# Kernel tuning notes

Hardware: AMD Instinct MI355X
Metric: run time of the kernel (lower is better)

Reference implementation:

```python
import jax, jax.numpy as jnp
import numpy as np

N_NODES = 100000


def _gat_conv(x, edge_index, W, att_src, att_dst, bias, concat):
    """PyG-style GATConv (eval mode, self-loops already in edge_index).
    x: [N, F_in], W: [F_in, H*C], att_*: [H, C], bias: [H*C] or [C].
    """
    N = x.shape[0]
    H, C = att_src.shape
    xl = (x @ W).reshape(N, H, C)                      # [N, H, C]
    a_src = jnp.einsum('nhc,hc->nh', xl, att_src)      # [N, H]
    a_dst = jnp.einsum('nhc,hc->nh', xl, att_dst)      # [N, H]
    src, dst = edge_index[0], edge_index[1]
    e = jax.nn.leaky_relu(a_src[src] + a_dst[dst], negative_slope=0.2)  # [E, H]
    # segment softmax over incoming edges per destination node
    e_max = jax.ops.segment_max(e, dst, num_segments=N)                 # [N, H]
    e_exp = jnp.exp(e - e_max[dst])                                     # [E, H]
    denom = jax.ops.segment_sum(e_exp, dst, num_segments=N)             # [N, H]
    alpha = e_exp / (denom[dst] + 1e-16)                                # [E, H]
    msg = xl[src] * alpha[:, :, None]                                   # [E, H, C]
    out = jax.ops.segment_sum(msg, dst, num_segments=N)                 # [N, H, C]
    out = out.reshape(N, H * C) if concat else out.mean(axis=1)
    return out + bias


def setup_inputs() -> dict:
    key = jax.random.key(0)
    ks = jax.random.split(key, 12)
    in_dim, hidden, heads, out_dim = 128, 16, 8, 64
    E = 1600000
    x = jax.random.normal(ks[0], (N_NODES, in_dim), dtype=jnp.float32)
    edge_index = jax.random.randint(ks[1], (2, E), 0, N_NODES, dtype=jnp.int32)
    s1 = 1.0 / np.sqrt(in_dim)
    s2 = 1.0 / np.sqrt(hidden * heads)
    return {
        'x': x,
        'edge_index': edge_index,
        'W1': jax.random.normal(ks[2], (in_dim, heads * hidden), dtype=jnp.float32) * s1,
        'att_src1': jax.random.normal(ks[3], (heads, hidden), dtype=jnp.float32) * 0.1,
        'att_dst1': jax.random.normal(ks[4], (heads, hidden), dtype=jnp.float32) * 0.1,
        'b1': jnp.zeros((heads * hidden,), dtype=jnp.float32),
        'W2': jax.random.normal(ks[5], (heads * hidden, out_dim), dtype=jnp.float32) * s2,
        'att_src2': jax.random.normal(ks[6], (1, out_dim), dtype=jnp.float32) * 0.1,
        'att_dst2': jax.random.normal(ks[7], (1, out_dim), dtype=jnp.float32) * 0.1,
        'b2': jnp.zeros((out_dim,), dtype=jnp.float32),
    }


def reference(x, edge_index, W1, att_src1, att_dst1, b1, W2, att_src2, att_dst2, b2):
    N = x.shape[0]
    # PyG GATConv default add_self_loops=True
    loops = jnp.tile(jnp.arange(N, dtype=edge_index.dtype), (2, 1))
    ei = jnp.concatenate([edge_index, loops], axis=1)
    h = _gat_conv(x, ei, W1, att_src1, att_dst1, b1, concat=True)
    h = jax.nn.elu(h)
    # dropout is identity in eval mode
    out = _gat_conv(h, ei, W2, att_src2, att_dst2, b2, concat=False)
    return out
```

## Files before the change

kernel.cpp:

```cpp
#include <hip/hip_runtime.h>
#include <cmath>

typedef _Float16 half8 __attribute__((ext_vector_type(8)));
typedef float f32x4 __attribute__((ext_vector_type(4)));

#define CAP 48

__device__ __forceinline__ float elu1(float v) {
    return v > 0.f ? v : (__expf(v) - 1.f);
}

__global__ __launch_bounds__(256) void k_scatter(
    const int* __restrict__ src, const int* __restrict__ dst,
    int* __restrict__ cnt, int* __restrict__ sorted, int E, int M, int npc)
{
    int color = blockIdx.x & 7;
    int lo = color * npc, hi = lo + npc;
    int nb = gridDim.x >> 3;
    size_t stride = (size_t)nb * 256;
    for (size_t e = (size_t)(blockIdx.x >> 3) * 256 + threadIdx.x; e < (size_t)M; e += stride) {
        int s, d;
        if (e < (size_t)E) { s = src[e]; d = dst[e]; } else { s = (int)(e - E); d = s; }
        if (d >= lo && d < hi) {
            int pos = atomicAdd(&cnt[d], 1);
            if (pos < CAP) sorted[(size_t)d * CAP + pos] = s;
        }
    }
}

__global__ __launch_bounds__(256) void k_gemm1(
    const float* __restrict__ x, const float* __restrict__ W,
    const float* __restrict__ att_s, const float* __restrict__ att_d,
    _Float16* __restrict__ xlh, float* __restrict__ a_s, float* __restrict__ a_d, int N)
{
    __shared__ _Float16 Wt[128 * 136];
    int t = threadIdx.x;
    for (int i = t; i < 128 * 128; i += 256) {
        int k = i >> 7, n = i & 127;
        Wt[n * 136 + k] = (_Float16)W[i];
    }
    __syncthreads();

    int wave = t >> 6, lane = t & 63;
    int cl = lane & 15, quad = lane >> 4;
    int arow = blockIdx.x * 64 + wave * 16 + cl;
    int rr = arow < N ? arow : N - 1;

    half8 af[4];
#pragma unroll
    for (int ks = 0; ks < 4; ks++) {
        const float4* p = (const float4*)(x + (size_t)rr * 128 + ks * 32 + quad * 8);
        float4 A = p[0], B = p[1];
        af[ks][0] = (_Float16)A.x; af[ks][1] = (_Float16)A.y;
        af[ks][2] = (_Float16)A.z; af[ks][3] = (_Float16)A.w;
        af[ks][4] = (_Float16)B.x; af[ks][5] = (_Float16)B.y;
        af[ks][6] = (_Float16)B.z; af[ks][7] = (_Float16)B.w;
    }

    f32x4 acc[8];
#pragma unroll
    for (int nt = 0; nt < 8; nt++) acc[nt] = (f32x4){0.f, 0.f, 0.f, 0.f};

#pragma unroll
    for (int nt = 0; nt < 8; nt++) {
        int n = nt * 16 + cl;
#pragma unroll
        for (int ks = 0; ks < 4; ks++) {
            half8 bf = *(const half8*)&Wt[n * 136 + ks * 32 + quad * 8];
            acc[nt] = __builtin_amdgcn_mfma_f32_16x16x32_f16(af[ks], bf, acc[nt], 0, 0, 0);
        }
    }

    float asl[8], adl[8];
#pragma unroll
    for (int nt = 0; nt < 8; nt++) {
        asl[nt] = att_s[nt * 16 + cl];
        adl[nt] = att_d[nt * 16 + cl];
    }

    int rbase = blockIdx.x * 64 + wave * 16 + quad * 4;
#pragma unroll
    for (int r = 0; r < 4; r++) {
        int orow = rbase + r;
        bool ok = orow < N;
#pragma unroll
        for (int nt = 0; nt < 8; nt++) {
            float v = acc[nt][r];
            if (ok) xlh[(size_t)orow * 128 + nt * 16 + cl] = (_Float16)v;
        }
#pragma unroll
        for (int nt = 0; nt < 8; nt++) {
            float ps = acc[nt][r] * asl[nt];
            float pd = acc[nt][r] * adl[nt];
            ps += __shfl_xor(ps, 1); ps += __shfl_xor(ps, 2);
            ps += __shfl_xor(ps, 4); ps += __shfl_xor(ps, 8);
            pd += __shfl_xor(pd, 1); pd += __shfl_xor(pd, 2);
            pd += __shfl_xor(pd, 4); pd += __shfl_xor(pd, 8);
            if (ok && cl == 0) {
                a_s[(size_t)orow * 8 + nt] = ps;
                a_d[(size_t)orow * 8 + nt] = pd;
            }
        }
    }
}

__global__ __launch_bounds__(256) void k_gemm2(
    const _Float16* __restrict__ h, const float* __restrict__ W,
    const float* __restrict__ att_s, const float* __restrict__ att_d,
    _Float16* __restrict__ xlh, float* __restrict__ a_s, float* __restrict__ a_d, int N)
{
    __shared__ _Float16 Wt[64 * 136];
    int t = threadIdx.x;
    for (int i = t; i < 128 * 64; i += 256) {
        int k = i >> 6, n = i & 63;
        Wt[n * 136 + k] = (_Float16)W[i];
    }
    __syncthreads();

    int wave = t >> 6, lane = t & 63;
    int cl = lane & 15, quad = lane >> 4;
    int arow = blockIdx.x * 64 + wave * 16 + cl;
    int rr = arow < N ? arow : N - 1;

    half8 af[4];
#pragma unroll
    for (int ks = 0; ks < 4; ks++)
        af[ks] = *(const half8*)(h + (size_t)rr * 128 + ks * 32 + quad * 8);

    f32x4 acc[4];
#pragma unroll
    for (int nt = 0; nt < 4; nt++) acc[nt] = (f32x4){0.f, 0.f, 0.f, 0.f};

#pragma unroll
    for (int nt = 0; nt < 4; nt++) {
        int n = nt * 16 + cl;
#pragma unroll
        for (int ks = 0; ks < 4; ks++) {
            half8 bf = *(const half8*)&Wt[n * 136 + ks * 32 + quad * 8];
            acc[nt] = __builtin_amdgcn_mfma_f32_16x16x32_f16(af[ks], bf, acc[nt], 0, 0, 0);
        }
    }

    float asl[4], adl[4];
#pragma unroll
    for (int nt = 0; nt < 4; nt++) {
        asl[nt] = att_s[nt * 16 + cl];
        adl[nt] = att_d[nt * 16 + cl];
    }

    int rbase = blockIdx.x * 64 + wave * 16 + quad * 4;
#pragma unroll
    for (int r = 0; r < 4; r++) {
        int orow = rbase + r;
        bool ok = orow < N;
        float ps = 0.f, pd = 0.f;
#pragma unroll
        for (int nt = 0; nt < 4; nt++) {
            float v = acc[nt][r];
            if (ok) xlh[(size_t)orow * 64 + nt * 16 + cl] = (_Float16)v;
            ps += v * asl[nt];
            pd += v * adl[nt];
        }
        ps += __shfl_xor(ps, 1); ps += __shfl_xor(ps, 2);
        ps += __shfl_xor(ps, 4); ps += __shfl_xor(ps, 8);
        pd += __shfl_xor(pd, 1); pd += __shfl_xor(pd, 2);
        pd += __shfl_xor(pd, 4); pd += __shfl_xor(pd, 8);
        if (ok && cl == 0) { a_s[orow] = ps; a_d[orow] = pd; }
    }
}

__global__ __launch_bounds__(256) void k_agg1(
    const int* __restrict__ cnt, const int* __restrict__ ss,
    const float* __restrict__ as, const float* __restrict__ ad,
    const _Float16* __restrict__ xlh, const float* __restrict__ b1,
    _Float16* __restrict__ h, int N)
{
    int t = threadIdx.x;
    int g = (blockIdx.x * 256 + t) >> 3;
    if (g >= N) return;
    int lane = t & 7;
    int c = lane * 16;
    int deg = cnt[g]; deg = deg < CAP ? deg : CAP;
    int start = g * CAP, end = start + deg;
    float adv = ad[(size_t)g * 8 + lane];

    float l = 0.f;
    float acc[16];
#pragma unroll
    for (int j = 0; j < 16; j++) acc[j] = 0.f;

    int i = start;
    for (; i + 2 <= end; i += 2) {
        int s0 = ss[i], s1 = ss[i + 1];
        float a0 = as[(size_t)s0 * 8 + lane];
        float a1 = as[(size_t)s1 * 8 + lane];
        const _Float16* p0 = xlh + (size_t)s0 * 128 + c;
        const _Float16* p1 = xlh + (size_t)s1 * 128 + c;
        half8 x0a = *(const half8*)p0, x0b = *(const half8*)(p0 + 8);
        half8 x1a = *(const half8*)p1, x1b = *(const half8*)(p1 + 8);
        float v0 = a0 + adv; v0 = v0 > 0.f ? v0 : 0.2f * v0;
        float v1 = a1 + adv; v1 = v1 > 0.f ? v1 : 0.2f * v1;
        float w0 = __expf(v0), w1 = __expf(v1);
        l += w0 + w1;
#pragma unroll
        for (int j = 0; j < 8; j++) {
            acc[j]     += (float)x0a[j] * w0 + (float)x1a[j] * w1;
            acc[j + 8] += (float)x0b[j] * w0 + (float)x1b[j] * w1;
        }
    }
    if (i < end) {
        int s0 = ss[i];
        float v0 = as[(size_t)s0 * 8 + lane] + adv;
        v0 = v0 > 0.f ? v0 : 0.2f * v0;
        float w0 = __expf(v0);
        l += w0;
        const _Float16* p0 = xlh + (size_t)s0 * 128 + c;
        half8 x0a = *(const half8*)p0, x0b = *(const half8*)(p0 + 8);
#pragma unroll
        for (int j = 0; j < 8; j++) {
            acc[j]     += (float)x0a[j] * w0;
            acc[j + 8] += (float)x0b[j] * w0;
        }
    }
    float inv = 1.f / (l + 1e-16f);
    float4 bq[4];
    bq[0] = *(const float4*)(b1 + c);
    bq[1] = *(const float4*)(b1 + c + 4);
    bq[2] = *(const float4*)(b1 + c + 8);
    bq[3] = *(const float4*)(b1 + c + 12);
    const float* bb = (const float*)bq;
    half8 o0, o1;
#pragma unroll
    for (int j = 0; j < 8; j++) {
        o0[j] = (_Float16)elu1(acc[j] * inv + bb[j]);
        o1[j] = (_Float16)elu1(acc[j + 8] * inv + bb[j + 8]);
    }
    *(half8*)(h + (size_t)g * 128 + c) = o0;
    *(half8*)(h + (size_t)g * 128 + c + 8) = o1;
}

__global__ __launch_bounds__(256) void k_agg2(
    const int* __restrict__ cnt, const int* __restrict__ ss,
    const float* __restrict__ as, const float* __restrict__ ad,
    const _Float16* __restrict__ xlh, const float* __restrict__ b2,
    float* __restrict__ out, int N)
{
    int t = threadIdx.x;
    int g = (blockIdx.x * 256 + t) >> 3;
    if (g >= N) return;
    int lane = t & 7;
    int c = lane * 8;
    int deg = cnt[g]; deg = deg < CAP ? deg : CAP;
    int start = g * CAP, end = start + deg;
    float adv = ad[g];

    float l = 0.f;
    float acc[8];
#pragma unroll
    for (int j = 0; j < 8; j++) acc[j] = 0.f;

    int i = start;
    for (; i + 4 <= end; i += 4) {
        int s0 = ss[i], s1 = ss[i + 1], s2 = ss[i + 2], s3 = ss[i + 3];
        float a0 = as[s0], a1 = as[s1], a2 = as[s2], a3 = as[s3];
        half8 x0 = *(const half8*)(xlh + (size_t)s0 * 64 + c);
        half8 x1 = *(const half8*)(xlh + (size_t)s1 * 64 + c);
        half8 x2 = *(const half8*)(xlh + (size_t)s2 * 64 + c);
        half8 x3 = *(const half8*)(xlh + (size_t)s3 * 64 + c);
        float v0 = a0 + adv; v0 = v0 > 0.f ? v0 : 0.2f * v0;
        float v1 = a1 + adv; v1 = v1 > 0.f ? v1 : 0.2f * v1;
        float v2 = a2 + adv; v2 = v2 > 0.f ? v2 : 0.2f * v2;
        float v3 = a3 + adv; v3 = v3 > 0.f ? v3 : 0.2f * v3;
        float w0 = __expf(v0), w1 = __expf(v1), w2 = __expf(v2), w3 = __expf(v3);
        l += (w0 + w1) + (w2 + w3);
#pragma unroll
        for (int j = 0; j < 8; j++)
            acc[j] += ((float)x0[j] * w0 + (float)x1[j] * w1)
                    + ((float)x2[j] * w2 + (float)x3[j] * w3);
    }
    for (; i < end; i++) {
        int s0 = ss[i];
        float v0 = as[s0] + adv;
        v0 = v0 > 0.f ? v0 : 0.2f * v0;
        float w0 = __expf(v0);
        l += w0;
        half8 x0 = *(const half8*)(xlh + (size_t)s0 * 64 + c);
#pragma unroll
        for (int j = 0; j < 8; j++) acc[j] += (float)x0[j] * w0;
    }
    float inv = 1.f / (l + 1e-16f);
    float4 b0 = *(const float4*)(b2 + c);
    float4 b4 = *(const float4*)(b2 + c + 4);
    float bb[8] = {b0.x, b0.y, b0.z, b0.w, b4.x, b4.y, b4.z, b4.w};
    float4 o0, o1;
    o0.x = acc[0] * inv + bb[0];
    o0.y = acc[1] * inv + bb[1];
    o0.z = acc[2] * inv + bb[2];
    o0.w = acc[3] * inv + bb[3];
    o1.x = acc[4] * inv + bb[4];
    o1.y = acc[5] * inv + bb[5];
    o1.z = acc[6] * inv + bb[6];
    o1.w = acc[7] * inv + bb[7];
    *(float4*)(out + (size_t)g * 64 + c) = o0;
    *(float4*)(out + (size_t)g * 64 + c + 4) = o1;
}

extern "C" void kernel_launch(void* const* d_in, const int* in_sizes, int n_in,
                              void* d_out, int out_size, void* d_ws, size_t ws_size,
                              hipStream_t stream) {
    const float* x   = (const float*)d_in[0];
    const int*   ei  = (const int*)  d_in[1];
    const float* W1  = (const float*)d_in[2];
    const float* as1 = (const float*)d_in[3];
    const float* ad1 = (const float*)d_in[4];
    const float* b1  = (const float*)d_in[5];
    const float* W2  = (const float*)d_in[6];
    const float* as2 = (const float*)d_in[7];
    const float* ad2 = (const float*)d_in[8];
    const float* b2  = (const float*)d_in[9];

    const int N = in_sizes[0] / 128;
    const int E = in_sizes[1] / 2;
    const int M = E + N;
    const int npc = (N + 7) / 8;
    const int SB = ((M + 256 * 8 - 1) / (256 * 8)) * 8;
    const int* src = ei;
    const int* dst = ei + E;

    float* ws    = (float*)d_ws;
    _Float16* xl1h = (_Float16*)ws;
    float* as1v  = ws   + (size_t)N * 64;
    float* ad1v  = as1v + (size_t)N * 8;
    _Float16* hbuf = (_Float16*)(ad1v + (size_t)N * 8);
    float* as2v  = ad1v + (size_t)N * 8 + (size_t)N * 64;
    float* ad2v  = as2v + (size_t)N;
    int*   cnt   = (int*)(ad2v + (size_t)N);
    int*   sorted= cnt + (size_t)N;
    _Float16* xl2h = xl1h;
    float* out   = (float*)d_out;

    size_t need = ((size_t)N * (147 + CAP)) * 4;
    if (ws_size < need) return;

    hipMemsetAsync(cnt, 0, (size_t)N * 4, stream);

    k_scatter<<<SB, 256, 0, stream>>>(src, dst, cnt, sorted, E, M, npc);
    k_gemm1  <<<(N + 63) / 64, 256, 0, stream>>>(x, W1, as1, ad1, xl1h, as1v, ad1v, N);

    k_agg1 <<<(int)(((size_t)N * 8 + 255) / 256), 256, 0, stream>>>(
        cnt, sorted, as1v, ad1v, xl1h, b1, hbuf, N);

    k_gemm2<<<(N + 63) / 64, 256, 0, stream>>>(hbuf, W2, as2, ad2, xl2h, as2v, ad2v, N);

    k_agg2 <<<(int)(((size_t)N * 8 + 255) / 256), 256, 0, stream>>>(
        cnt, sorted, as2v, ad2v, xl2h, b2, out, N);
}
```

Before: 350.4 us.

## Fuse layer-1 aggregation with layer-2 GEMM and fold counter reset into GEMM1

The layer-1 aggregation now writes its ELU output tile into shared memory, and the same block immediately runs the layer-2 MFMA projection and attention dot products. This removes the global round trip of the hidden activations and one kernel launch. The separate memset of the degree counters is replaced by zeroing inside k_gemm1, which now runs before the scatter. The cost is that every 32-node block reloads and converts W2 into LDS, and the fused kernel uses more LDS per block, which may lower occupancy for the latency-bound gather loop.

```diff
diff --git a/kernel.cpp b/kernel.cpp
--- a/kernel.cpp
+++ b/kernel.cpp
@@ -8,6 +8,86 @@
 
 __device__ __forceinline__ float elu1(float v) {
     return v > 0.f ? v : (__expf(v) - 1.f);
+}
+
+__global__ __launch_bounds__(256) void k_gemm1(
+    const float* __restrict__ x, const float* __restrict__ W,
+    const float* __restrict__ att_s, const float* __restrict__ att_d,
+    _Float16* __restrict__ xlh, float* __restrict__ a_s, float* __restrict__ a_d,
+    int* __restrict__ cnt, int N)
+{
+    __shared__ _Float16 Wt[128 * 136];
+    int t = threadIdx.x;
+
+    for (int i = blockIdx.x * 256 + t; i < N; i += gridDim.x * 256) cnt[i] = 0;
+
+    for (int i = t; i < 128 * 128; i += 256) {
+        int k = i >> 7, n = i & 127;
+        Wt[n * 136 + k] = (_Float16)W[i];
+    }
+    __syncthreads();
+
+    int wave = t >> 6, lane = t & 63;
+    int cl = lane & 15, quad = lane >> 4;
+    int arow = blockIdx.x * 64 + wave * 16 + cl;
+    int rr = arow < N ? arow : N - 1;
+
+    half8 af[4];
+#pragma unroll
+    for (int ks = 0; ks < 4; ks++) {
+        const float4* p = (const float4*)(x + (size_t)rr * 128 + ks * 32 + quad * 8);
+        float4 A = p[0], B = p[1];
+        af[ks][0] = (_Float16)A.x; af[ks][1] = (_Float16)A.y;
+        af[ks][2] = (_Float16)A.z; af[ks][3] = (_Float16)A.w;
+        af[ks][4] = (_Float16)B.x; af[ks][5] = (_Float16)B.y;
+        af[ks][6] = (_Float16)B.z; af[ks][7] = (_Float16)B.w;
+    }
+
+    f32x4 acc[8];
+#pragma unroll
+    for (int nt = 0; nt < 8; nt++) acc[nt] = (f32x4){0.f, 0.f, 0.f, 0.f};
+
+#pragma unroll
+    for (int nt = 0; nt < 8; nt++) {
+        int n = nt * 16 + cl;
+#pragma unroll
+        for (int ks = 0; ks < 4; ks++) {
+            half8 bf = *(const half8*)&Wt[n * 136 + ks * 32 + quad * 8];
+            acc[nt] = __builtin_amdgcn_mfma_f32_16x16x32_f16(af[ks], bf, acc[nt], 0, 0, 0);
+        }
+    }
+
+    float asl[8], adl[8];
+#pragma unroll
+    for (int nt = 0; nt < 8; nt++) {
+        asl[nt] = att_s[nt * 16 + cl];
+        adl[nt] = att_d[nt * 16 + cl];
+    }
+
+    int rbase = blockIdx.x * 64 + wave * 16 + quad * 4;
+#pragma unroll
+    for (int r = 0; r < 4; r++) {
+        int orow = rbase + r;
+        bool ok = orow < N;
+#pragma unroll
+        for (int nt = 0; nt < 8; nt++) {
+            float v = acc[nt][r];
+            if (ok) xlh[(size_t)orow * 128 + nt * 16 + cl] = (_Float16)v;
+        }
+#pragma unroll
+        for (int nt = 0; nt < 8; nt++) {
+            float ps = acc[nt][r] * asl[nt];
+            float pd = acc[nt][r] * adl[nt];
+            ps += __shfl_xor(ps, 1); ps += __shfl_xor(ps, 2);
+            ps += __shfl_xor(ps, 4); ps += __shfl_xor(ps, 8);
+            pd += __shfl_xor(pd, 1); pd += __shfl_xor(pd, 2);
+            pd += __shfl_xor(pd, 4); pd += __shfl_xor(pd, 8);
+            if (ok && cl == 0) {
+                a_s[(size_t)orow * 8 + nt] = ps;
+                a_d[(size_t)orow * 8 + nt] = pd;
+            }
+        }
+    }
 }
 
 __global__ __launch_bounds__(256) void k_scatter(
@@ -28,215 +108,144 @@
     }
 }
 
-__global__ __launch_bounds__(256) void k_gemm1(
-    const float* __restrict__ x, const float* __restrict__ W,
-    const float* __restrict__ att_s, const float* __restrict__ att_d,
-    _Float16* __restrict__ xlh, float* __restrict__ a_s, float* __restrict__ a_d, int N)
+__global__ __launch_bounds__(256) void k_agg1_gemm2(
+    const int* __restrict__ cnt, const int* __restrict__ ss,
+    const float* __restrict__ as, const float* __restrict__ ad,
+    const _Float16* __restrict__ xlh, const float* __restrict__ b1,
+    const float* __restrict__ W2,
+    const float* __restrict__ att_s2, const float* __restrict__ att_d2,
+    _Float16* __restrict__ xl2h, float* __restrict__ a_s2, float* __restrict__ a_d2, int N)
 {
-    __shared__ _Float16 Wt[128 * 136];
+    __shared__ _Float16 W2t[64 * 136];
+    __shared__ _Float16 Ht[32 * 136];
+    __shared__ float asb[2][32], adb[2][32];
+
     int t = threadIdx.x;
-    for (int i = t; i < 128 * 128; i += 256) {
-        int k = i >> 7, n = i & 127;
-        Wt[n * 136 + k] = (_Float16)W[i];
+
+    for (int i = t; i < 128 * 64; i += 256) {
+        int k = i >> 6, n = i & 63;
+        W2t[n * 136 + k] = (_Float16)W2[i];
+    }
+
+    int ln = t >> 3;
+    int g = blockIdx.x * 32 + ln;
+    int lane8 = t & 7;
+    int c = lane8 * 16;
+    {
+        int gg = g < N ? g : N - 1;
+        int deg = cnt[gg]; deg = deg < CAP ? deg : CAP;
+        int start = gg * CAP, end = start + deg;
+        float adv = ad[(size_t)gg * 8 + lane8];
+
+        float l = 0.f;
+        float acc[16];
+#pragma unroll
+        for (int j = 0; j < 16; j++) acc[j] = 0.f;
+
+        int i = start;
+        for (; i + 2 <= end; i += 2) {
+            int s0 = ss[i], s1 = ss[i + 1];
+            float a0 = as[(size_t)s0 * 8 + lane8];
+            float a1 = as[(size_t)s1 * 8 + lane8];
+            const _Float16* p0 = xlh + (size_t)s0 * 128 + c;
+            const _Float16* p1 = xlh + (size_t)s1 * 128 + c;
+            half8 x0a = *(const half8*)p0, x0b = *(const half8*)(p0 + 8);
+            half8 x1a = *(const half8*)p1, x1b = *(const half8*)(p1 + 8);
+            float v0 = a0 + adv; v0 = v0 > 0.f ? v0 : 0.2f * v0;
+            float v1 = a1 + adv; v1 = v1 > 0.f ? v1 : 0.2f * v1;
+            float w0 = __expf(v0), w1 = __expf(v1);
+            l += w0 + w1;
+#pragma unroll
+            for (int j = 0; j < 8; j++) {
+                acc[j]     += (float)x0a[j] * w0 + (float)x1a[j] * w1;
+                acc[j + 8] += (float)x0b[j] * w0 + (float)x1b[j] * w1;
+            }
+        }
+        if (i < end) {
+            int s0 = ss[i];
+            float v0 = as[(size_t)s0 * 8 + lane8] + adv;
+            v0 = v0 > 0.f ? v0 : 0.2f * v0;
+            float w0 = __expf(v0);
+            l += w0;
+            const _Float16* p0 = xlh + (size_t)s0 * 128 + c;
+            half8 x0a = *(const half8*)p0, x0b = *(const half8*)(p0 + 8);
+#pragma unroll
+            for (int j = 0; j < 8; j++) {
+                acc[j]     += (float)x0a[j] * w0;
+                acc[j + 8] += (float)x0b[j] * w0;
+            }
+        }
+        float inv = 1.f / (l + 1e-16f);
+        float4 bq[4];
+        bq[0] = *(const float4*)(b1 + c);
+        bq[1] = *(const float4*)(b1 + c + 4);
+        bq[2] = *(const float4*)(b1 + c + 8);
+        bq[3] = *(const float4*)(b1 + c + 12);
+        const float* bb = (const float*)bq;
+        half8 o0, o1;
+#pragma unroll
+        for (int j = 0; j < 8; j++) {
+            o0[j] = (_Float16)elu1(acc[j] * inv + bb[j]);
+            o1[j] = (_Float16)elu1(acc[j + 8] * inv + bb[j + 8]);
+        }
+        *(half8*)&Ht[ln * 136 + c] = o0;
+        *(half8*)&Ht[ln * 136 + c + 8] = o1;
     }
     __syncthreads();
 
     int wave = t >> 6, lane = t & 63;
     int cl = lane & 15, quad = lane >> 4;
-    int arow = blockIdx.x * 64 + wave * 16 + cl;
-    int rr = arow < N ? arow : N - 1;
+    int rt = wave >> 1;
+    int half = wave & 1;
 
     half8 af[4];
 #pragma unroll
-    for (int ks = 0; ks < 4; ks++) {
-        const float4* p = (const float4*)(x + (size_t)rr * 128 + ks * 32 + quad * 8);
-        float4 A = p[0], B = p[1];
-        af[ks][0] = (_Float16)A.x; af[ks][1] = (_Float16)A.y;
-        af[ks][2] = (_Float16)A.z; af[ks][3] = (_Float16)A.w;
-        af[ks][4] = (_Float16)B.x; af[ks][5] = (_Float16)B.y;
-        af[ks][6] = (_Float16)B.z; af[ks][7] = (_Float16)B.w;
-    }
-
-    f32x4 acc[8];
-#pragma unroll
-    for (int nt = 0; nt < 8; nt++) acc[nt] = (f32x4){0.f, 0.f, 0.f, 0.f};
-
-#pragma unroll
-    for (int nt = 0; nt < 8; nt++) {
-        int n = nt * 16 + cl;
+    for (int ks = 0; ks < 4; ks++)
+        af[ks] = *(const half8*)&Ht[(rt * 16 + cl) * 136 + ks * 32 + quad * 8];
+
+    f32x4 acc2[2];
+    acc2[0] = (f32x4){0.f, 0.f, 0.f, 0.f};
+    acc2[1] = (f32x4){0.f, 0.f, 0.f, 0.f};
+    float asl[2], adl[2];
+#pragma unroll
+    for (int ntl = 0; ntl < 2; ntl++) {
+        int n = (half * 2 + ntl) * 16 + cl;
+        asl[ntl] = att_s2[n];
+        adl[ntl] = att_d2[n];
 #pragma unroll
         for (int ks = 0; ks < 4; ks++) {
-            half8 bf = *(const half8*)&Wt[n * 136 + ks * 32 + quad * 8];
-            acc[nt] = __builtin_amdgcn_mfma_f32_16x16x32_f16(af[ks], bf, acc[nt], 0, 0, 0);
-        }
-    }
-
-    float asl[8], adl[8];
-#pragma unroll
-    for (int nt = 0; nt < 8; nt++) {
-        asl[nt] = att_s[nt * 16 + cl];
-        adl[nt] = att_d[nt * 16 + cl];
-    }
-
-    int rbase = blockIdx.x * 64 + wave * 16 + quad * 4;
+            half8 bf = *(const half8*)&W2t[n * 136 + ks * 32 + quad * 8];
+            acc2[ntl] = __builtin_amdgcn_mfma_f32_16x16x32_f16(af[ks], bf, acc2[ntl], 0, 0, 0);
+        }
+    }
+
 #pragma unroll
     for (int r = 0; r < 4; r++) {
-        int orow = rbase + r;
-        bool ok = orow < N;
-#pragma unroll
-        for (int nt = 0; nt < 8; nt++) {
-            float v = acc[nt][r];
-            if (ok) xlh[(size_t)orow * 128 + nt * 16 + cl] = (_Float16)v;
-        }
-#pragma unroll
-        for (int nt = 0; nt < 8; nt++) {
-            float ps = acc[nt][r] * asl[nt];
-            float pd = acc[nt][r] * adl[nt];
-            ps += __shfl_xor(ps, 1); ps += __shfl_xor(ps, 2);
-            ps += __shfl_xor(ps, 4); ps += __shfl_xor(ps, 8);
-            pd += __shfl_xor(pd, 1); pd += __shfl_xor(pd, 2);
-            pd += __shfl_xor(pd, 4); pd += __shfl_xor(pd, 8);
-            if (ok && cl == 0) {
-                a_s[(size_t)orow * 8 + nt] = ps;
-                a_d[(size_t)orow * 8 + nt] = pd;
-            }
-        }
-    }
-}
-
-__global__ __launch_bounds__(256) void k_gemm2(
-    const _Float16* __restrict__ h, const float* __restrict__ W,
-    const float* __restrict__ att_s, const float* __restrict__ att_d,
-    _Float16* __restrict__ xlh, float* __restrict__ a_s, float* __restrict__ a_d, int N)
-{
-    __shared__ _Float16 Wt[64 * 136];
-    int t = threadIdx.x;
-    for (int i = t; i < 128 * 64; i += 256) {
-        int k = i >> 6, n = i & 63;
-        Wt[n * 136 + k] = (_Float16)W[i];
-    }
-    __syncthreads();
-
-    int wave = t >> 6, lane = t & 63;
-    int cl = lane & 15, quad = lane >> 4;
-    int arow = blockIdx.x * 64 + wave * 16 + cl;
-    int rr = arow < N ? arow : N - 1;
-
-    half8 af[4];
-#pragma unroll
-    for (int ks = 0; ks < 4; ks++)
-        af[ks] = *(const half8*)(h + (size_t)rr * 128 + ks * 32 + quad * 8);
-
-    f32x4 acc[4];
-#pragma unroll
-    for (int nt = 0; nt < 4; nt++) acc[nt] = (f32x4){0.f, 0.f, 0.f, 0.f};
-
-#pragma unroll
-    for (int nt = 0; nt < 4; nt++) {
-        int n = nt * 16 + cl;
-#pragma unroll
-        for (int ks = 0; ks < 4; ks++) {
-            half8 bf = *(const half8*)&Wt[n * 136 + ks * 32 + quad * 8];
-            acc[nt] = __builtin_amdgcn_mfma_f32_16x16x32_f16(af[ks], bf, acc[nt], 0, 0, 0);
-        }
-    }
-
-    float asl[4], adl[4];
-#pragma unroll
-    for (int nt = 0; nt < 4; nt++) {
-        asl[nt] = att_s[nt * 16 + cl];
-        adl[nt] = att_d[nt * 16 + cl];
-    }
-
-    int rbase = blockIdx.x * 64 + wave * 16 + quad * 4;
-#pragma unroll
-    for (int r = 0; r < 4; r++) {
-        int orow = rbase + r;
+        int lrow = rt * 16 + quad * 4 + r;
+        int orow = blockIdx.x * 32 + lrow;
         bool ok = orow < N;
         float ps = 0.f, pd = 0.f;
 #pragma unroll
-        for (int nt = 0; nt < 4; nt++) {
-            float v = acc[nt][r];
-            if (ok) xlh[(size_t)orow * 64 + nt * 16 + cl] = (_Float16)v;
-            ps += v * asl[nt];
-            pd += v * adl[nt];
+        for (int ntl = 0; ntl < 2; ntl++) {
+            float v = acc2[ntl][r];
+            if (ok) xl2h[(size_t)orow * 64 + (half * 2 + ntl) * 16 + cl] = (_Float16)v;
+            ps += v * asl[ntl];
+            pd += v * adl[ntl];
         }
         ps += __shfl_xor(ps, 1); ps += __shfl_xor(ps, 2);
         ps += __shfl_xor(ps, 4); ps += __shfl_xor(ps, 8);
         pd += __shfl_xor(pd, 1); pd += __shfl_xor(pd, 2);
         pd += __shfl_xor(pd, 4); pd += __shfl_xor(pd, 8);
-        if (ok && cl == 0) { a_s[orow] = ps; a_d[orow] = pd; }
-    }
-}
-
-__global__ __launch_bounds__(256) void k_agg1(
-    const int* __restrict__ cnt, const int* __restrict__ ss,
-    const float* __restrict__ as, const float* __restrict__ ad,
-    const _Float16* __restrict__ xlh, const float* __restrict__ b1,
-    _Float16* __restrict__ h, int N)
-{
-    int t = threadIdx.x;
-    int g = (blockIdx.x * 256 + t) >> 3;
-    if (g >= N) return;
-    int lane = t & 7;
-    int c = lane * 16;
-    int deg = cnt[g]; deg = deg < CAP ? deg : CAP;
-    int start = g * CAP, end = start + deg;
-    float adv = ad[(size_t)g * 8 + lane];
-
-    float l = 0.f;
-    float acc[16];
-#pragma unroll
-    for (int j = 0; j < 16; j++) acc[j] = 0.f;
-
-    int i = start;
-    for (; i + 2 <= end; i += 2) {
-        int s0 = ss[i], s1 = ss[i + 1];
-        float a0 = as[(size_t)s0 * 8 + lane];
-        float a1 = as[(size_t)s1 * 8 + lane];
-        const _Float16* p0 = xlh + (size_t)s0 * 128 + c;
-        const _Float16* p1 = xlh + (size_t)s1 * 128 + c;
-        half8 x0a = *(const half8*)p0, x0b = *(const half8*)(p0 + 8);
-        half8 x1a = *(const half8*)p1, x1b = *(const half8*)(p1 + 8);
-        float v0 = a0 + adv; v0 = v0 > 0.f ? v0 : 0.2f * v0;
-        float v1 = a1 + adv; v1 = v1 > 0.f ? v1 : 0.2f * v1;
-        float w0 = __expf(v0), w1 = __expf(v1);
-        l += w0 + w1;
-#pragma unroll
-        for (int j = 0; j < 8; j++) {
-            acc[j]     += (float)x0a[j] * w0 + (float)x1a[j] * w1;
-            acc[j + 8] += (float)x0b[j] * w0 + (float)x1b[j] * w1;
-        }
-    }
-    if (i < end) {
-        int s0 = ss[i];
-        float v0 = as[(size_t)s0 * 8 + lane] + adv;
-        v0 = v0 > 0.f ? v0 : 0.2f * v0;
-        float w0 = __expf(v0);
-        l += w0;
-        const _Float16* p0 = xlh + (size_t)s0 * 128 + c;
-        half8 x0a = *(const half8*)p0, x0b = *(const half8*)(p0 + 8);
-#pragma unroll
-        for (int j = 0; j < 8; j++) {
-            acc[j]     += (float)x0a[j] * w0;
-            acc[j + 8] += (float)x0b[j] * w0;
-        }
-    }
-    float inv = 1.f / (l + 1e-16f);
-    float4 bq[4];
-    bq[0] = *(const float4*)(b1 + c);
-    bq[1] = *(const float4*)(b1 + c + 4);
-    bq[2] = *(const float4*)(b1 + c + 8);
-    bq[3] = *(const float4*)(b1 + c + 12);
-    const float* bb = (const float*)bq;
-    half8 o0, o1;
-#pragma unroll
-    for (int j = 0; j < 8; j++) {
-        o0[j] = (_Float16)elu1(acc[j] * inv + bb[j]);
-        o1[j] = (_Float16)elu1(acc[j + 8] * inv + bb[j + 8]);
-    }
-    *(half8*)(h + (size_t)g * 128 + c) = o0;
-    *(half8*)(h + (size_t)g * 128 + c + 8) = o1;
+        if (cl == 0) { asb[half][lrow] = ps; adb[half][lrow] = pd; }
+    }
+    __syncthreads();
+    if (t < 32) {
+        int orow = blockIdx.x * 32 + t;
+        if (orow < N) {
+            a_s2[orow] = asb[0][t] + asb[1][t];
+            a_d2[orow] = adb[0][t] + adb[1][t];
+        }
+    }
 }
 
 __global__ __launch_bounds__(256) void k_agg2(
@@ -331,26 +340,21 @@
     _Float16* xl1h = (_Float16*)ws;
     float* as1v  = ws   + (size_t)N * 64;
     float* ad1v  = as1v + (size_t)N * 8;
-    _Float16* hbuf = (_Float16*)(ad1v + (size_t)N * 8);
-    float* as2v  = ad1v + (size_t)N * 8 + (size_t)N * 64;
+    _Float16* xl2h = (_Float16*)(ad1v + (size_t)N * 8);
+    float* as2v  = ad1v + (size_t)N * 8 + (size_t)N * 32;
     float* ad2v  = as2v + (size_t)N;
     int*   cnt   = (int*)(ad2v + (size_t)N);
     int*   sorted= cnt + (size_t)N;
-    _Float16* xl2h = xl1h;
     float* out   = (float*)d_out;
 
-    size_t need = ((size_t)N * (147 + CAP)) * 4;
+    size_t need = ((size_t)N * (115 + CAP)) * 4;
     if (ws_size < need) return;
 
-    hipMemsetAsync(cnt, 0, (size_t)N * 4, stream);
-
+    k_gemm1  <<<(N + 63) / 64, 256, 0, stream>>>(x, W1, as1, ad1, xl1h, as1v, ad1v, cnt, N);
     k_scatter<<<SB, 256, 0, stream>>>(src, dst, cnt, sorted, E, M, npc);
-    k_gemm1  <<<(N + 63) / 64, 256, 0, stream>>>(x, W1, as1, ad1, xl1h, as1v, ad1v, N);
-
-    k_agg1 <<<(int)(((size_t)N * 8 + 255) / 256), 256, 0, stream>>>(
-        cnt, sorted, as1v, ad1v, xl1h, b1, hbuf, N);
-
-    k_gemm2<<<(N + 63) / 64, 256, 0, stream>>>(hbuf, W2, as2, ad2, xl2h, as2v, ad2v, N);
+
+    k_agg1_gemm2<<<(N + 31) / 32, 256, 0, stream>>>(
+        cnt, sorted, as1v, ad1v, xl1h, b1, W2, as2, ad2, xl2h, as2v, ad2v, N);
 
     k_agg2 <<<(int)(((size_t)N * 8 + 255) / 256), 256, 0, stream>>>(
         cnt, sorted, as2v, ad2v, xl2h, b2, out, N);
```

Result: no change. 343.8 us (-1.9%).
